# Kernel tuning notes

Measured on AMD Instinct MI355X. Metric: run time of the kernel, lower is better.

The kernel has to match this reference:

```python
import jax, jax.numpy as jnp
import numpy as np

N_NODES = 50000
N_EDGES = 1000000
HID = 64
L = 3
EPS_MSG = 1e-7   # GENConv message eps
EPS_SM = 1e-16   # PyG scatter-softmax denominator eps
LN_EPS = 1e-5


def layernorm(x, g, b):
    mu = jnp.mean(x, axis=-1, keepdims=True)
    var = jnp.var(x, axis=-1, keepdims=True)
    return (x - mu) * jax.lax.rsqrt(var + LN_EPS) * g + b


def genconv(x, src, dst, edge_attr, t, W1, b1, g1, be1, W2, b2):
    # message: relu(x_j + e_ij) + eps  -> [E, HID]
    msg = jax.nn.relu(x[src] + edge_attr) + EPS_MSG
    # softmax aggregation over incoming edges of each dst node
    logits = msg * t
    m = jax.ops.segment_max(logits, dst, num_segments=N_NODES)
    m = jnp.where(jnp.isfinite(m), m, 0.0)
    e = jnp.exp(logits - m[dst])
    s = jax.ops.segment_sum(e, dst, num_segments=N_NODES) + EPS_SM
    agg = jax.ops.segment_sum((e / s[dst]) * msg, dst, num_segments=N_NODES)
    # root residual + MLP [64 -> 128 -> 64]
    h = agg + x
    h = h @ W1 + b1
    h = jax.nn.relu(layernorm(h, g1, be1))
    return h @ W2 + b2


def setup_inputs() -> dict:
    key = jax.random.key(0)
    ks = jax.random.split(key, 10)
    inp = {
        'x': jax.random.normal(ks[0], (N_NODES, 16), jnp.float32),
        'edge_attr': jax.random.uniform(ks[1], (N_EDGES, 1), jnp.float32),
        'edge_index': jax.random.randint(ks[2], (2, N_EDGES), 0, N_NODES, jnp.int32),
        'W_node': jax.random.normal(ks[3], (16, HID), jnp.float32) / np.sqrt(16.0),
        'b_node': jnp.zeros((HID,), jnp.float32),
        'W_edge': jax.random.normal(ks[4], (1, HID), jnp.float32),
        'b_edge': jnp.zeros((HID,), jnp.float32),
        't': jnp.ones((L,), jnp.float32),
        'W1': jax.random.normal(ks[5], (L, HID, 2 * HID), jnp.float32) / np.sqrt(float(HID)),
        'b1': jnp.zeros((L, 2 * HID), jnp.float32),
        'ln_g': jnp.ones((L, 2 * HID), jnp.float32),
        'ln_b': jnp.zeros((L, 2 * HID), jnp.float32),
        'W2': jax.random.normal(ks[6], (L, 2 * HID, HID), jnp.float32) / np.sqrt(2.0 * HID),
        'b2': jnp.zeros((L, HID), jnp.float32),
        'norm_g': jnp.ones((L, HID), jnp.float32),
        'norm_b': jnp.zeros((L, HID), jnp.float32),
        'W_lin': jax.random.normal(ks[7], (HID, 64), jnp.float32) / np.sqrt(float(HID)),
        'b_lin': jnp.zeros((64,), jnp.float32),
    }
    return inp


def reference(x, edge_attr, edge_index, W_node, b_node, W_edge, b_edge, t,
              W1, b1, ln_g, ln_b, W2, b2, norm_g, norm_b, W_lin, b_lin):
    src, dst = edge_index[0], edge_index[1]
    h = x @ W_node + b_node                 # [N, HID]
    ea = edge_attr @ W_edge + b_edge        # [E, HID]
    # layer 0: conv only
    h = genconv(h, src, dst, ea, t[0], W1[0], b1[0], ln_g[0], ln_b[0], W2[0], b2[0])
    # layers 1..L-1: res+ blocks (norm -> relu -> conv -> residual); dropout is identity in eval
    for i in range(1, L):
        z = jax.nn.relu(layernorm(h, norm_g[i], norm_b[i]))
        h = h + genconv(z, src, dst, ea, t[i], W1[i], b1[i], ln_g[i], ln_b[i], W2[i], b2[i])
    # final norm/act reuses layer 0's norm
    h = jax.nn.relu(layernorm(h, norm_g[0], norm_b[0]))
    # adaptive avg/max pool (N, 64) -> (1, 32): pool over all nodes, channel bins of 2
    avg = h.mean(axis=0).reshape(32, 2).mean(axis=1)
    mx = h.max(axis=0).reshape(32, 2).max(axis=1)
    emb = jnp.concatenate([avg, mx])[None, :]   # [1, 64]
    return emb @ W_lin + b_lin                  # [1, 64]
```

## Files before the change

### kernel.cpp

```cpp
#include <hip/hip_runtime.h>
#include <math.h>

#define N_NODES 50000
#define N_EDGES 1000000
#define HID 64
#define CAP 64
#define N_TILES (N_NODES / 16)
#define NB_MLP 512
#define VB_S 72
#define UB_S 136
#define NB_ENC ((N_NODES + 3) / 4)
#define NB_WPREP ((3 * 8192 + 255) / 256)
#define NBK 196
#define BKCAP 6144
#define EPB 4096
#define NB1 ((N_EDGES + EPB - 1) / EPB)
static_assert(N_NODES % 16 == 0, "tile math");
static_assert(N_NODES <= 65536, "src must fit in 16 bits");

typedef __attribute__((ext_vector_type(8))) short short8;
typedef __attribute__((ext_vector_type(4))) float f32x4;

__device__ __forceinline__ unsigned short f2bf(float x) {
    unsigned u = __float_as_uint(x);
    u += 0x7FFFu + ((u >> 16) & 1u);
    return (unsigned short)(u >> 16);
}
__device__ __forceinline__ float bfbits_hi(unsigned pk) {
    return __uint_as_float(pk & 0xFFFF0000u);
}
__device__ __forceinline__ float bf2f(unsigned short v) {
    return __uint_as_float(((unsigned)v) << 16);
}
__device__ __forceinline__ unsigned addpk(unsigned a, unsigned b) {
    float lo = __uint_as_float(a << 16) + __uint_as_float(b << 16);
    float hi = __uint_as_float(a & 0xFFFF0000u) + __uint_as_float(b & 0xFFFF0000u);
    return (unsigned)f2bf(lo) | ((unsigned)f2bf(hi) << 16);
}

__global__ __launch_bounds__(256) void k_front(
    const float* __restrict__ x, const float* __restrict__ Wn,
    const float* __restrict__ bn, unsigned short* __restrict__ zb,
    const float* __restrict__ W1, const float* __restrict__ W2,
    unsigned short* __restrict__ w1p, unsigned short* __restrict__ w2p) {
    int b = blockIdx.x;
    if (b < NB_ENC) {
        int n = b * 4 + (threadIdx.x >> 6);
        int c = threadIdx.x & 63;
        if (n >= N_NODES) return;
        float acc = bn[c];
        const float* xr = x + n * 16;
        #pragma unroll
        for (int k = 0; k < 16; ++k) acc = fmaf(xr[k], Wn[k * 64 + c], acc);
        zb[n * 64 + c] = f2bf(acc);
    } else {
        int i = (b - NB_ENC) * 256 + threadIdx.x;
        if (i >= 3 * 8192) return;
        int L = i >> 13, r = i & 8191;
        int j = r & 7, lane = (r >> 3) & 63;
        int quad = lane >> 4, col = lane & 15;
        {
            int st = r >> 9;
            int s = st >> 3, t = st & 7;
            w1p[i] = f2bf(W1[L * 8192 + (s * 32 + quad * 8 + j) * 128 + t * 16 + col]);
        }
        {
            int ft = r >> 9;
            int s = ft >> 2, t = ft & 3;
            w2p[i] = f2bf(W2[L * 8192 + (s * 32 + quad * 8 + j) * 64 + t * 16 + col]);
        }
    }
}

__global__ __launch_bounds__(256) void k_bin1(
    const int* __restrict__ ei, const float* __restrict__ eattr,
    int* __restrict__ gcnt, uint2* __restrict__ coarse) {
    __shared__ unsigned pk_l[EPB];
    __shared__ unsigned short dst_l[EPB];
    __shared__ unsigned spk[EPB];
    __shared__ unsigned short sdst[EPB];
    __shared__ int hist[NBK], loc[NBK], gbase[NBK], cur[NBK];
    __shared__ int inc[256];
    int tid = threadIdx.x;
    int e0 = blockIdx.x * EPB;
    int nel = N_EDGES - e0; if (nel > EPB) nel = EPB;
    for (int b = tid; b < NBK; b += 256) { hist[b] = 0; cur[b] = 0; }
    __syncthreads();
    for (int j = tid; j < nel; j += 256) {
        int i = e0 + j;
        int d = ei[N_EDGES + i];
        unsigned pk = ((unsigned)f2bf(eattr[i]) << 16) | (unsigned)(ei[i] & 0xFFFF);
        pk_l[j] = pk; dst_l[j] = (unsigned short)d;
        atomicAdd(&hist[d >> 8], 1);
    }
    __syncthreads();
    int v = (tid < NBK) ? hist[tid] : 0;
    inc[tid] = v;
    __syncthreads();
    #pragma unroll
    for (int dd = 1; dd < 256; dd <<= 1) {
        int t2 = (tid >= dd) ? inc[tid - dd] : 0;
        __syncthreads();
        inc[tid] += t2;
        __syncthreads();
    }
    if (tid < NBK) {
        loc[tid] = inc[tid] - v;
        gbase[tid] = atomicAdd(&gcnt[tid], v);
    }
    __syncthreads();
    for (int j = tid; j < nel; j += 256) {
        int bkt = dst_l[j] >> 8;
        int r = atomicAdd(&cur[bkt], 1);
        int pos = loc[bkt] + r;
        spk[pos] = pk_l[j]; sdst[pos] = dst_l[j];
    }
    __syncthreads();
    for (int j = tid; j < nel; j += 256) {
        int d = sdst[j];
        int bkt = d >> 8;
        int off = gbase[bkt] + (j - loc[bkt]);
        if (off < BKCAP) coarse[(size_t)bkt * BKCAP + off] = make_uint2(spk[j], (unsigned)d);
    }
}

__global__ __launch_bounds__(256) void k_bin2(
    const int* __restrict__ gcnt, const uint2* __restrict__ coarse,
    int* __restrict__ cnt, unsigned int* __restrict__ s_pack) {
    __shared__ unsigned epk[BKCAP];
    __shared__ unsigned char eln[BKCAP];
    __shared__ unsigned spk[BKCAP];
    __shared__ unsigned char sln[BKCAP];
    __shared__ int hist[256], cur[256], inc2[256];
    int tid = threadIdx.x;
    int b = blockIdx.x;
    int m = gcnt[b]; if (m > BKCAP) m = BKCAP;
    hist[tid] = 0; cur[tid] = 0;
    __syncthreads();
    for (int j = tid; j < m; j += 256) {
        uint2 e = coarse[(size_t)b * BKCAP + j];
        epk[j] = e.x;
        int ln = (int)(e.y & 255u);
        eln[j] = (unsigned char)ln;
        atomicAdd(&hist[ln], 1);
    }
    __syncthreads();
    int v = hist[tid];
    inc2[tid] = v;
    __syncthreads();
    #pragma unroll
    for (int dd = 1; dd < 256; dd <<= 1) {
        int t2 = (tid >= dd) ? inc2[tid - dd] : 0;
        __syncthreads();
        inc2[tid] += t2;
        __syncthreads();
    }
    int lv = inc2[tid] - v;
    __syncthreads();
    hist[tid] = lv;
    int node = b * 256 + tid;
    if (node < N_NODES) cnt[node] = v;
    __syncthreads();
    for (int j = tid; j < m; j += 256) {
        int ln = eln[j];
        int r = atomicAdd(&cur[ln], 1);
        int pos = hist[ln] + r;
        spk[pos] = epk[j]; sln[pos] = (unsigned char)ln;
    }
    __syncthreads();
    for (int j = tid; j < m; j += 256) {
        int ln = sln[j];
        int k = j - hist[ln];
        if (k < CAP) s_pack[(size_t)(b * 256 + ln) * CAP + k] = spk[j];
    }
}

__global__ __launch_bounds__(256) void k_agg(
    const unsigned short* __restrict__ zb, const int* __restrict__ cnt,
    const unsigned int* __restrict__ s_pack,
    const float* __restrict__ We, const float* __restrict__ be,
    const float* __restrict__ t, int layer, unsigned short* __restrict__ aggb) {
    int wid = (blockIdx.x * blockDim.x + threadIdx.x) >> 6;
    int lane = threadIdx.x & 63;
    if (wid >= N_NODES) return;
    int deg = cnt[wid];
    deg = (deg < CAP) ? deg : CAP;
    int beg = wid * CAP, end = beg + deg;
    int half = lane >> 5;
    int c2 = lane & 31;
    float we0 = We[2 * c2], we1 = We[2 * c2 + 1];
    float bv0 = be[2 * c2], bv1 = be[2 * c2 + 1];
    float tl = t[layer];
    const unsigned* zbu = (const unsigned*)zb;
    float s0 = 0.f, s1 = 0.f, n0 = 0.f, n1 = 0.f;
    int i = beg;
    for (; i + 7 < end; i += 8) {
        unsigned pk[4];
        #pragma unroll
        for (int j = 0; j < 4; ++j) {
            unsigned pa = s_pack[i + 2 * j];
            unsigned pb = s_pack[i + 2 * j + 1];
            pk[j] = half ? pb : pa;
        }
        unsigned zu[4];
        #pragma unroll
        for (int j = 0; j < 4; ++j) zu[j] = zbu[(pk[j] & 0xFFFFu) * 32 + c2];
        #pragma unroll
        for (int j = 0; j < 4; ++j) {
            float ea = bfbits_hi(pk[j]);
            float z0 = __uint_as_float(zu[j] << 16);
            float z1 = __uint_as_float(zu[j] & 0xFFFF0000u);
            float m0 = fmaxf(z0 + fmaf(ea, we0, bv0), 0.f) + 1e-7f;
            float m1 = fmaxf(z1 + fmaf(ea, we1, bv1), 0.f) + 1e-7f;
            float p0 = __expf(m0 * tl), p1 = __expf(m1 * tl);
            s0 += p0; n0 = fmaf(p0, m0, n0);
            s1 += p1; n1 = fmaf(p1, m1, n1);
        }
    }
    for (; i + 1 < end; i += 2) {
        unsigned pa = s_pack[i], pb = s_pack[i + 1];
        unsigned pk = half ? pb : pa;
        unsigned zu = zbu[(pk & 0xFFFFu) * 32 + c2];
        float ea = bfbits_hi(pk);
        float z0 = __uint_as_float(zu << 16);
        float z1 = __uint_as_float(zu & 0xFFFF0000u);
        float m0 = fmaxf(z0 + fmaf(ea, we0, bv0), 0.f) + 1e-7f;
        float m1 = fmaxf(z1 + fmaf(ea, we1, bv1), 0.f) + 1e-7f;
        float p0 = __expf(m0 * tl), p1 = __expf(m1 * tl);
        s0 += p0; n0 = fmaf(p0, m0, n0);
        s1 += p1; n1 = fmaf(p1, m1, n1);
    }
    if (i < end) {
        unsigned pk = s_pack[i];
        unsigned zu = zbu[(pk & 0xFFFFu) * 32 + c2];
        float ea = bfbits_hi(pk);
        float z0 = __uint_as_float(zu << 16);
        float z1 = __uint_as_float(zu & 0xFFFF0000u);
        float m0 = fmaxf(z0 + fmaf(ea, we0, bv0), 0.f) + 1e-7f;
        float m1 = fmaxf(z1 + fmaf(ea, we1, bv1), 0.f) + 1e-7f;
        float p0 = __expf(m0 * tl), p1 = __expf(m1 * tl);
        if (half == 0) {
            s0 += p0; n0 = fmaf(p0, m0, n0);
            s1 += p1; n1 = fmaf(p1, m1, n1);
        }
    }
    s0 += __shfl_xor(s0, 32, 64); n0 += __shfl_xor(n0, 32, 64);
    s1 += __shfl_xor(s1, 32, 64); n1 += __shfl_xor(n1, 32, 64);
    if (half == 0) {
        unsigned r = (unsigned)f2bf(n0 / (s0 + 1e-16f)) |
                     ((unsigned)f2bf(n1 / (s1 + 1e-16f)) << 16);
        ((unsigned*)aggb)[wid * 32 + c2] = r;
    }
}

__global__ __launch_bounds__(256) void k_mlp(
    const unsigned short* __restrict__ aggb, unsigned short* __restrict__ zb,
    unsigned short* __restrict__ hb,
    const unsigned short* __restrict__ w1p, const unsigned short* __restrict__ w2p,
    const float* __restrict__ b1,
    const float* __restrict__ g1, const float* __restrict__ be1,
    const float* __restrict__ b2,
    const float* __restrict__ ng, const float* __restrict__ nb, int mode,
    float* __restrict__ pb_sum, float* __restrict__ pb_max) {
    __shared__ unsigned short w1s[8192];
    __shared__ unsigned short w2s[8192];
    __shared__ unsigned short vbuf[4][16 * VB_S];
    __shared__ unsigned short ubuf[4][16 * UB_S];
    __shared__ float lssum[4][4][16], lsmax[4][4][16];
    int lane = threadIdx.x & 63;
    int wave = threadIdx.x >> 6;
    int col = lane & 15, quad = lane >> 4;
    unsigned short* vb = vbuf[wave];
    unsigned short* ub = ubuf[wave];

    {
        const uint4* s1 = (const uint4*)w1p;
        const uint4* s2 = (const uint4*)w2p;
        uint4* d1 = (uint4*)w1s;
        uint4* d2 = (uint4*)w2s;
        #pragma unroll
        for (int i = 0; i < 4; ++i) {
            d1[threadIdx.x + i * 256] = s1[threadIdx.x + i * 256];
            d2[threadIdx.x + i * 256] = s2[threadIdx.x + i * 256];
        }
    }
    __syncthreads();

    float b1f[8], g1f[8], e1f[8];
    #pragma unroll
    for (int t = 0; t < 8; ++t) {
        int ch = t * 16 + col;
        b1f[t] = b1[ch]; g1f[t] = g1[ch]; e1f[t] = be1[ch];
    }
    float b2f_[4], ngf[4], nbf[4];
    #pragma unroll
    for (int t = 0; t < 4; ++t) {
        b2f_[t] = b2[t * 16 + col];
        ngf[t] = ng[t * 16 + col];
        nbf[t] = nb[t * 16 + col];
    }

    float psum[4] = {0.f, 0.f, 0.f, 0.f};
    float pmax[4] = {0.f, 0.f, 0.f, 0.f};
    int nd = lane >> 2;
    int cg = (lane & 3) * 16;

    for (int tile = blockIdx.x * 4 + wave; tile < N_TILES; tile += NB_MLP * 4) {
        int n0 = tile * 16;
        const uint4* ap = (const uint4*)(aggb + (size_t)(n0 + nd) * 64 + cg);
        const uint4* zp = (const uint4*)(zb + (size_t)(n0 + nd) * 64 + cg);
        uint4 a0 = ap[0], a1 = ap[1], z0 = zp[0], z1 = zp[1];
        uint4 r0, r1;
        r0.x = addpk(a0.x, z0.x); r0.y = addpk(a0.y, z0.y);
        r0.z = addpk(a0.z, z0.z); r0.w = addpk(a0.w, z0.w);
        r1.x = addpk(a1.x, z1.x); r1.y = addpk(a1.y, z1.y);
        r1.z = addpk(a1.z, z1.z); r1.w = addpk(a1.w, z1.w);
        uint4* vdst = (uint4*)&vb[nd * VB_S + cg];
        vdst[0] = r0;
        vdst[1] = r1;

        short8 af0 = *(const short8*)&vb[col * VB_S + quad * 8];
        short8 af1 = *(const short8*)&vb[col * VB_S + 32 + quad * 8];

        uint4 h0, h1;
        if (mode >= 1) {
            const uint4* hp = (const uint4*)(hb + (size_t)(n0 + nd) * 64 + cg);
            h0 = hp[0]; h1 = hp[1];
        }

        f32x4 au[8];
        #pragma unroll
        for (int t = 0; t < 8; ++t) {
            short8 w0 = *(const short8*)&w1s[((0 * 8 + t) * 64 + lane) * 8];
            short8 w1 = *(const short8*)&w1s[((1 * 8 + t) * 64 + lane) * 8];
            f32x4 c = {0.f, 0.f, 0.f, 0.f};
            c = __builtin_amdgcn_mfma_f32_16x16x32_bf16(af0, w0, c, 0, 0, 0);
            c = __builtin_amdgcn_mfma_f32_16x16x32_bf16(af1, w1, c, 0, 0, 0);
            au[t] = c;
        }
        #pragma unroll
        for (int r = 0; r < 4; ++r) {
            float sx = 0.f, sq = 0.f;
            #pragma unroll
            for (int t = 0; t < 8; ++t) {
                float v = au[t][r] + b1f[t];
                sx += v; sq += v * v;
            }
            #pragma unroll
            for (int mask = 1; mask < 16; mask <<= 1) {
                sx += __shfl_xor(sx, mask, 64);
                sq += __shfl_xor(sq, mask, 64);
            }
            float mu = sx * (1.f / 128.f);
            float var = sq * (1.f / 128.f) - mu * mu;
            float rs = rsqrtf(var + 1e-5f);
            int row = quad * 4 + r;
            #pragma unroll
            for (int t = 0; t < 8; ++t) {
                float v = au[t][r] + b1f[t];
                float y = fmaxf(fmaf((v - mu) * rs, g1f[t], e1f[t]), 0.f);
                ub[row * UB_S + t * 16 + col] = f2bf(y);
            }
        }
        f32x4 oc[4];
        #pragma unroll
        for (int t = 0; t < 4; ++t) oc[t] = (f32x4){0.f, 0.f, 0.f, 0.f};
        #pragma unroll
        for (int s = 0; s < 4; ++s) {
            short8 a = *(const short8*)&ub[col * UB_S + s * 32 + quad * 8];
            #pragma unroll
            for (int t = 0; t < 4; ++t) {
                short8 w = *(const short8*)&w2s[((s * 4 + t) * 64 + lane) * 8];
                oc[t] = __builtin_amdgcn_mfma_f32_16x16x32_bf16(a, w, oc[t], 0, 0, 0);
            }
        }
        if (mode >= 1) {
            uint4* hdst = (uint4*)&vb[nd * VB_S + cg];
            hdst[0] = h0;
            hdst[1] = h1;
        }
        #pragma unroll
        for (int r = 0; r < 4; ++r) {
            int row = quad * 4 + r;
            float val[4];
            #pragma unroll
            for (int t = 0; t < 4; ++t) {
                val[t] = oc[t][r] + b2f_[t];
                if (mode >= 1) val[t] += bf2f(vb[row * VB_S + t * 16 + col]);
            }
            float sx = 0.f, sq = 0.f;
            #pragma unroll
            for (int t = 0; t < 4; ++t) { sx += val[t]; sq += val[t] * val[t]; }
            #pragma unroll
            for (int mask = 1; mask < 16; mask <<= 1) {
                sx += __shfl_xor(sx, mask, 64);
                sq += __shfl_xor(sq, mask, 64);
            }
            float mu = sx * (1.f / 64.f);
            float var = sq * (1.f / 64.f) - mu * mu;
            float rs = rsqrtf(var + 1e-5f);
            #pragma unroll
            for (int t = 0; t < 4; ++t) {
                float y = fmaxf(fmaf((val[t] - mu) * rs, ngf[t], nbf[t]), 0.f);
                if (mode <= 1) {
                    vb[row * VB_S + t * 16 + col] = f2bf(val[t]);
                    ub[row * UB_S + t * 16 + col] = f2bf(y);
                } else {
                    psum[t] += y;
                    pmax[t] = fmaxf(pmax[t], y);
                }
            }
        }
        if (mode <= 1) {
            const uint4* hsrc = (const uint4*)&vb[nd * VB_S + cg];
            const uint4* zsrc = (const uint4*)&ub[nd * UB_S + cg];
            uint4* hdst = (uint4*)(hb + (size_t)(n0 + nd) * 64 + cg);
            uint4* zdst = (uint4*)(zb + (size_t)(n0 + nd) * 64 + cg);
            hdst[0] = hsrc[0]; hdst[1] = hsrc[1];
            zdst[0] = zsrc[0]; zdst[1] = zsrc[1];
        }
    }
    if (mode == 2) {
        #pragma unroll
        for (int t = 0; t < 4; ++t) {
            psum[t] += __shfl_xor(psum[t], 16, 64);
            psum[t] += __shfl_xor(psum[t], 32, 64);
            pmax[t] = fmaxf(pmax[t], __shfl_xor(pmax[t], 16, 64));
            pmax[t] = fmaxf(pmax[t], __shfl_xor(pmax[t], 32, 64));
        }
        if (quad == 0) {
            #pragma unroll
            for (int t = 0; t < 4; ++t) {
                lssum[wave][t][col] = psum[t];
                lsmax[wave][t][col] = pmax[t];
            }
        }
        __syncthreads();
        if (wave == 0) {
            int t = lane >> 4, c = lane & 15;
            float s = lssum[0][t][c] + lssum[1][t][c] + lssum[2][t][c] + lssum[3][t][c];
            float mx = fmaxf(fmaxf(lsmax[0][t][c], lsmax[1][t][c]),
                             fmaxf(lsmax[2][t][c], lsmax[3][t][c]));
            pb_sum[blockIdx.x * 64 + lane] = s;
            pb_max[blockIdx.x * 64 + lane] = mx;
        }
    }
}

__global__ __launch_bounds__(1024) void k_head(
    const float* __restrict__ pb_sum, const float* __restrict__ pb_max,
    const float* __restrict__ Wl, const float* __restrict__ bl, float* __restrict__ out) {
    __shared__ float sa4[16][64], sm4[16][64];
    __shared__ float sa[64], sm[64], emb[64];
    int t = threadIdx.x;
    int ch = t & 63, part = t >> 6;
    float s = 0.f, mx = 0.f;
    for (int b = part; b < NB_MLP; b += 16) {
        s += pb_sum[b * 64 + ch];
        mx = fmaxf(mx, pb_max[b * 64 + ch]);
    }
    sa4[part][ch] = s; sm4[part][ch] = mx;
    __syncthreads();
    if (t < 64) {
        float ss = 0.f, mm = 0.f;
        #pragma unroll
        for (int q = 0; q < 16; ++q) {
            ss += sa4[q][t];
            mm = fmaxf(mm, sm4[q][t]);
        }
        sa[t] = ss; sm[t] = mm;
    }
    __syncthreads();
    if (t < 64) {
        if (t < 32) {
            emb[t] = (sa[2 * t] + sa[2 * t + 1]) * (0.5f / (float)N_NODES);
        } else {
            int i = t - 32;
            emb[t] = fmaxf(sm[2 * i], sm[2 * i + 1]);
        }
    }
    __syncthreads();
    if (t < 64) {
        float acc = bl[t];
        for (int k = 0; k < 64; ++k) acc = fmaf(emb[k], Wl[k * 64 + t], acc);
        out[t] = acc;
    }
}

extern "C" void kernel_launch(void* const* d_in, const int* in_sizes, int n_in,
                              void* d_out, int out_size, void* d_ws, size_t ws_size,
                              hipStream_t stream) {
    const float* x     = (const float*)d_in[0];
    const float* eattr = (const float*)d_in[1];
    const int*   ei    = (const int*)d_in[2];
    const float* Wn    = (const float*)d_in[3];
    const float* bn    = (const float*)d_in[4];
    const float* We    = (const float*)d_in[5];
    const float* be    = (const float*)d_in[6];
    const float* t     = (const float*)d_in[7];
    const float* W1    = (const float*)d_in[8];
    const float* b1    = (const float*)d_in[9];
    const float* lg    = (const float*)d_in[10];
    const float* lb    = (const float*)d_in[11];
    const float* W2    = (const float*)d_in[12];
    const float* b2    = (const float*)d_in[13];
    const float* ng    = (const float*)d_in[14];
    const float* nb    = (const float*)d_in[15];
    const float* Wl    = (const float*)d_in[16];
    const float* bl    = (const float*)d_in[17];
    float* out = (float*)d_out;

    char* p = (char*)d_ws;
    unsigned short* hb   = (unsigned short*)p; p += (size_t)N_NODES * 64 * 2;
    unsigned short* zb   = (unsigned short*)p; p += (size_t)N_NODES * 64 * 2;
    unsigned short* aggb = (unsigned short*)p; p += (size_t)N_NODES * 64 * 2;
    unsigned int* s_pack = (unsigned int*)p; p += (size_t)N_NODES * CAP * 4;
    int* cnt    = (int*)p;  p += (size_t)N_NODES * 4;
    int* gcnt   = (int*)p;  p += (size_t)256 * 4;
    uint2* coarse = (uint2*)p; p += (size_t)NBK * BKCAP * 8;
    float* pb_sum = (float*)p; p += (size_t)NB_MLP * 64 * 4;
    float* pb_max = (float*)p; p += (size_t)NB_MLP * 64 * 4;
    unsigned short* w1p = (unsigned short*)p; p += (size_t)3 * 8192 * 2;
    unsigned short* w2p = (unsigned short*)p; p += (size_t)3 * 8192 * 2;

    hipMemsetAsync(gcnt, 0, (size_t)NBK * sizeof(int), stream);

    k_front<<<NB_ENC + NB_WPREP, 256, 0, stream>>>(x, Wn, bn, zb, W1, W2, w1p, w2p);
    k_bin1<<<NB1, 256, 0, stream>>>(ei, eattr, gcnt, coarse);
    k_bin2<<<NBK, 256, 0, stream>>>(gcnt, coarse, cnt, s_pack);

    k_agg<<<(N_NODES + 3) / 4, 256, 0, stream>>>(zb, cnt, s_pack, We, be, t, 0, aggb);
    k_mlp<<<NB_MLP, 256, 0, stream>>>(aggb, zb, hb, w1p, w2p, b1, lg, lb, b2,
                                      ng + 64, nb + 64, 0, pb_sum, pb_max);
    k_agg<<<(N_NODES + 3) / 4, 256, 0, stream>>>(zb, cnt, s_pack, We, be, t, 1, aggb);
    k_mlp<<<NB_MLP, 256, 0, stream>>>(aggb, zb, hb, w1p + 8192, w2p + 8192,
                                      b1 + 128, lg + 128, lb + 128, b2 + 64,
                                      ng + 128, nb + 128, 1, pb_sum, pb_max);
    k_agg<<<(N_NODES + 3) / 4, 256, 0, stream>>>(zb, cnt, s_pack, We, be, t, 2, aggb);
    k_mlp<<<NB_MLP, 256, 0, stream>>>(aggb, zb, hb, w1p + 2 * 8192, w2p + 2 * 8192,
                                      b1 + 2 * 128, lg + 2 * 128, lb + 2 * 128, b2 + 2 * 64,
                                      ng, nb, 2, pb_sum, pb_max);

    k_head<<<1, 1024, 0, stream>>>(pb_sum, pb_max, Wl, bl, out);
}
```

Before: 297.5 us.

## Merge edge binning into front kernel, unroll aggregation by 16, raise MLP grid

The first-pass edge binning kernel is folded into k_front as extra blocks, so binning, node encoding and weight packing run in one launch. The aggregation loop gains a 16-edge unrolled stage ahead of the 8-edge one, giving more gathers in flight per wave. The MLP grid grows from 512 to 782 blocks. The aim is to remove a launch and let independent front work overlap, but k_front now reserves about 33KB of shared memory for every block, including the encoding blocks, which may lower occupancy for that part.

```diff
diff --git a/kernel.cpp b/kernel.cpp
--- a/kernel.cpp
+++ b/kernel.cpp
@@ -6,7 +6,7 @@
 #define HID 64
 #define CAP 64
 #define N_TILES (N_NODES / 16)
-#define NB_MLP 512
+#define NB_MLP 782
 #define VB_S 72
 #define UB_S 136
 #define NB_ENC ((N_NODES + 3) / 4)
@@ -42,10 +42,60 @@
     const float* __restrict__ x, const float* __restrict__ Wn,
     const float* __restrict__ bn, unsigned short* __restrict__ zb,
     const float* __restrict__ W1, const float* __restrict__ W2,
-    unsigned short* __restrict__ w1p, unsigned short* __restrict__ w2p) {
+    unsigned short* __restrict__ w1p, unsigned short* __restrict__ w2p,
+    const int* __restrict__ ei, const float* __restrict__ eattr,
+    int* __restrict__ gcnt, uint2* __restrict__ coarse) {
+    __shared__ unsigned pk_l[EPB];
+    __shared__ unsigned short dst_l[EPB];
+    __shared__ unsigned spk[EPB];
+    __shared__ unsigned short sdst[EPB];
+    __shared__ int hist[NBK], loc[NBK], gbase[NBK], cur[NBK];
+    __shared__ int inc[256];
     int b = blockIdx.x;
-    if (b < NB_ENC) {
-        int n = b * 4 + (threadIdx.x >> 6);
+    if (b < NB1) {
+        int tid = threadIdx.x;
+        int e0 = b * EPB;
+        int nel = N_EDGES - e0; if (nel > EPB) nel = EPB;
+        for (int q = tid; q < NBK; q += 256) { hist[q] = 0; cur[q] = 0; }
+        __syncthreads();
+        for (int j = tid; j < nel; j += 256) {
+            int i = e0 + j;
+            int d = ei[N_EDGES + i];
+            unsigned pk = ((unsigned)f2bf(eattr[i]) << 16) | (unsigned)(ei[i] & 0xFFFF);
+            pk_l[j] = pk; dst_l[j] = (unsigned short)d;
+            atomicAdd(&hist[d >> 8], 1);
+        }
+        __syncthreads();
+        int v = (tid < NBK) ? hist[tid] : 0;
+        inc[tid] = v;
+        __syncthreads();
+        #pragma unroll
+        for (int dd = 1; dd < 256; dd <<= 1) {
+            int t2 = (tid >= dd) ? inc[tid - dd] : 0;
+            __syncthreads();
+            inc[tid] += t2;
+            __syncthreads();
+        }
+        if (tid < NBK) {
+            loc[tid] = inc[tid] - v;
+            gbase[tid] = atomicAdd(&gcnt[tid], v);
+        }
+        __syncthreads();
+        for (int j = tid; j < nel; j += 256) {
+            int bkt = dst_l[j] >> 8;
+            int r = atomicAdd(&cur[bkt], 1);
+            int pos = loc[bkt] + r;
+            spk[pos] = pk_l[j]; sdst[pos] = dst_l[j];
+        }
+        __syncthreads();
+        for (int j = tid; j < nel; j += 256) {
+            int d = sdst[j];
+            int bkt = d >> 8;
+            int off = gbase[bkt] + (j - loc[bkt]);
+            if (off < BKCAP) coarse[(size_t)bkt * BKCAP + off] = make_uint2(spk[j], (unsigned)d);
+        }
+    } else if (b < NB1 + NB_ENC) {
+        int n = (b - NB1) * 4 + (threadIdx.x >> 6);
         int c = threadIdx.x & 63;
         if (n >= N_NODES) return;
         float acc = bn[c];
@@ -54,7 +104,7 @@
         for (int k = 0; k < 16; ++k) acc = fmaf(xr[k], Wn[k * 64 + c], acc);
         zb[n * 64 + c] = f2bf(acc);
     } else {
-        int i = (b - NB_ENC) * 256 + threadIdx.x;
+        int i = (b - NB1 - NB_ENC) * 256 + threadIdx.x;
         if (i >= 3 * 8192) return;
         int L = i >> 13, r = i & 8191;
         int j = r & 7, lane = (r >> 3) & 63;
@@ -69,58 +119,6 @@
             int s = ft >> 2, t = ft & 3;
             w2p[i] = f2bf(W2[L * 8192 + (s * 32 + quad * 8 + j) * 64 + t * 16 + col]);
         }
-    }
-}
-
-__global__ __launch_bounds__(256) void k_bin1(
-    const int* __restrict__ ei, const float* __restrict__ eattr,
-    int* __restrict__ gcnt, uint2* __restrict__ coarse) {
-    __shared__ unsigned pk_l[EPB];
-    __shared__ unsigned short dst_l[EPB];
-    __shared__ unsigned spk[EPB];
-    __shared__ unsigned short sdst[EPB];
-    __shared__ int hist[NBK], loc[NBK], gbase[NBK], cur[NBK];
-    __shared__ int inc[256];
-    int tid = threadIdx.x;
-    int e0 = blockIdx.x * EPB;
-    int nel = N_EDGES - e0; if (nel > EPB) nel = EPB;
-    for (int b = tid; b < NBK; b += 256) { hist[b] = 0; cur[b] = 0; }
-    __syncthreads();
-    for (int j = tid; j < nel; j += 256) {
-        int i = e0 + j;
-        int d = ei[N_EDGES + i];
-        unsigned pk = ((unsigned)f2bf(eattr[i]) << 16) | (unsigned)(ei[i] & 0xFFFF);
-        pk_l[j] = pk; dst_l[j] = (unsigned short)d;
-        atomicAdd(&hist[d >> 8], 1);
-    }
-    __syncthreads();
-    int v = (tid < NBK) ? hist[tid] : 0;
-    inc[tid] = v;
-    __syncthreads();
-    #pragma unroll
-    for (int dd = 1; dd < 256; dd <<= 1) {
-        int t2 = (tid >= dd) ? inc[tid - dd] : 0;
-        __syncthreads();
-        inc[tid] += t2;
-        __syncthreads();
-    }
-    if (tid < NBK) {
-        loc[tid] = inc[tid] - v;
-        gbase[tid] = atomicAdd(&gcnt[tid], v);
-    }
-    __syncthreads();
-    for (int j = tid; j < nel; j += 256) {
-        int bkt = dst_l[j] >> 8;
-        int r = atomicAdd(&cur[bkt], 1);
-        int pos = loc[bkt] + r;
-        spk[pos] = pk_l[j]; sdst[pos] = dst_l[j];
-    }
-    __syncthreads();
-    for (int j = tid; j < nel; j += 256) {
-        int d = sdst[j];
-        int bkt = d >> 8;
-        int off = gbase[bkt] + (j - loc[bkt]);
-        if (off < BKCAP) coarse[(size_t)bkt * BKCAP + off] = make_uint2(spk[j], (unsigned)d);
     }
 }
 
@@ -194,6 +192,29 @@
     const unsigned* zbu = (const unsigned*)zb;
     float s0 = 0.f, s1 = 0.f, n0 = 0.f, n1 = 0.f;
     int i = beg;
+    for (; i + 15 < end; i += 16) {
+        unsigned pk[8];
+        #pragma unroll
+        for (int j = 0; j < 8; ++j) {
+            unsigned pa = s_pack[i + 2 * j];
+            unsigned pb = s_pack[i + 2 * j + 1];
+            pk[j] = half ? pb : pa;
+        }
+        unsigned zu[8];
+        #pragma unroll
+        for (int j = 0; j < 8; ++j) zu[j] = zbu[(pk[j] & 0xFFFFu) * 32 + c2];
+        #pragma unroll
+        for (int j = 0; j < 8; ++j) {
+            float ea = bfbits_hi(pk[j]);
+            float z0 = __uint_as_float(zu[j] << 16);
+            float z1 = __uint_as_float(zu[j] & 0xFFFF0000u);
+            float m0 = fmaxf(z0 + fmaf(ea, we0, bv0), 0.f) + 1e-7f;
+            float m1 = fmaxf(z1 + fmaf(ea, we1, bv1), 0.f) + 1e-7f;
+            float p0 = __expf(m0 * tl), p1 = __expf(m1 * tl);
+            s0 += p0; n0 = fmaf(p0, m0, n0);
+            s1 += p1; n1 = fmaf(p1, m1, n1);
+        }
+    }
     for (; i + 7 < end; i += 8) {
         unsigned pk[4];
         #pragma unroll
@@ -525,8 +546,8 @@
 
     hipMemsetAsync(gcnt, 0, (size_t)NBK * sizeof(int), stream);
 
-    k_front<<<NB_ENC + NB_WPREP, 256, 0, stream>>>(x, Wn, bn, zb, W1, W2, w1p, w2p);
-    k_bin1<<<NB1, 256, 0, stream>>>(ei, eattr, gcnt, coarse);
+    k_front<<<NB1 + NB_ENC + NB_WPREP, 256, 0, stream>>>(
+        x, Wn, bn, zb, W1, W2, w1p, w2p, ei, eattr, gcnt, coarse);
     k_bin2<<<NBK, 256, 0, stream>>>(gcnt, coarse, cnt, s_pack);
 
     k_agg<<<(N_NODES + 3) / 4, 256, 0, stream>>>(zb, cnt, s_pack, We, be, t, 0, aggb);
```

Result: no change. 299.3 us (+0.6%).
